# Optimization experiments

Measured on AMD Instinct MI355X. Metric: run time of the kernel, lower is better.

## Reference

```python
import jax, jax.numpy as jnp
import numpy as np

H, C = 4, 32            # heads, per-head channels
HID = H * C             # 128
IN_DIM, OUT_DIM = 300, 4
N, E = 50000, 800000
TE = HID // H           # time-encode dim = 32
EDGE_DIM = 2 * TE + 3   # 67
L = 2                   # num_layers


def setup_inputs() -> dict:
    key = jax.random.key(0)
    ks = jax.random.split(key, 20)
    p = lambda k, shape: jax.random.normal(k, shape, jnp.float32) * 0.02
    return {
        "x": jax.random.normal(ks[0], (N, IN_DIM), jnp.float32),
        "ei_td": jax.random.randint(ks[1], (2, E), 0, N),
        "ei_bu": jax.random.randint(ks[2], (2, E), 0, N),
        "ea_td": jax.random.uniform(ks[3], (E, 4), jnp.float32),
        "ea_bu": jax.random.uniform(ks[4], (E, 4), jnp.float32),
        "W_in": p(ks[5], (IN_DIM, HID)), "b_in": jnp.zeros((HID,), jnp.float32),
        "te_w": jax.random.uniform(ks[6], (TE,), jnp.float32),
        # stacked TransformerConv params: [layer, etype(TD,BU), ...]
        "Wq": p(ks[7], (L, 2, HID, HID)), "bq": jnp.zeros((L, 2, HID), jnp.float32),
        "Wk": p(ks[8], (L, 2, HID, HID)), "bk": jnp.zeros((L, 2, HID), jnp.float32),
        "Wv": p(ks[9], (L, 2, HID, HID)), "bv": jnp.zeros((L, 2, HID), jnp.float32),
        "We": p(ks[10], (L, 2, EDGE_DIM, HID)),  # lin_edge has no bias in PyG
        "Wskip": p(ks[11], (L, 2, HID, HID)), "bskip": jnp.zeros((L, 2, HID), jnp.float32),
        "gamma": jnp.ones((L, HID), jnp.float32), "beta": jnp.zeros((L, HID), jnp.float32),
        "W_out": p(ks[12], ((L + 1) * HID, OUT_DIM)), "b_out": jnp.zeros((OUT_DIM,), jnp.float32),
        "W_dec": p(ks[13], (HID, IN_DIM)), "b_dec": jnp.zeros((IN_DIM,), jnp.float32),
    }


def _edge_enc(ea, te_w):
    # TimeEncode on dt_norm, then [sin, cos, w_norm, infl_flag, cos_sim]
    ft = ea[:, 1:2] * te_w  # [E, TE]
    return jnp.concatenate([jnp.sin(ft), jnp.cos(ft), ea[:, 0:1], ea[:, 2:3], ea[:, 3:4]], axis=1)


def _tconv(h, src, dst, enc, Wq, bq, Wk, bk, Wv, bv, We, Wskip, bskip):
    # PyG TransformerConv (concat=True, root_weight=True, beta=False)
    n = h.shape[0]
    q = (h @ Wq + bq).reshape(n, H, C)
    k = (h @ Wk + bk).reshape(n, H, C)
    v = (h @ Wv + bv).reshape(n, H, C)
    e = (enc @ We).reshape(-1, H, C)                 # per-edge key/value offset
    ke = k[src] + e                                  # [E,H,C]
    alpha = jnp.einsum('ehc,ehc->eh', q[dst], ke) / jnp.sqrt(jnp.float32(C))
    amax = jax.ops.segment_max(alpha, dst, num_segments=n)     # scatter-softmax
    ex = jnp.exp(alpha - amax[dst])
    den = jax.ops.segment_sum(ex, dst, num_segments=n)
    a = ex / (den[dst] + 1e-16)                      # [E,H]
    msg = (v[src] + e) * a[:, :, None]
    out = jax.ops.segment_sum(msg, dst, num_segments=n).reshape(n, HID)
    return out + h @ Wskip + bskip                   # root/skip connection


def _ln(x, g, b):
    mu = jnp.mean(x, axis=-1, keepdims=True)
    var = jnp.mean((x - mu) ** 2, axis=-1, keepdims=True)
    return (x - mu) / jnp.sqrt(var + 1e-5) * g + b


def reference(x, ei_td, ei_bu, ea_td, ea_bu, W_in, b_in, te_w,
              Wq, bq, Wk, bk, Wv, bv, We, Wskip, bskip,
              gamma, beta, W_out, b_out, W_dec, b_dec):
    h = jax.nn.relu(x @ W_in + b_in)
    outs = [h]
    enc_td = _edge_enc(ea_td, te_w)
    enc_bu = _edge_enc(ea_bu, te_w)
    for i in range(L):
        o_td = _tconv(h, ei_td[0], ei_td[1], enc_td,
                      Wq[i, 0], bq[i, 0], Wk[i, 0], bk[i, 0], Wv[i, 0], bv[i, 0],
                      We[i, 0], Wskip[i, 0], bskip[i, 0])
        o_bu = _tconv(h, ei_bu[0], ei_bu[1], enc_bu,
                      Wq[i, 1], bq[i, 1], Wk[i, 1], bk[i, 1], Wv[i, 1], bv[i, 1],
                      We[i, 1], Wskip[i, 1], bskip[i, 1])
        t = jax.nn.relu(o_td + o_bu)                 # HeteroConv aggr='sum'; dropout=eval noop
        h = _ln(t, gamma[i], beta[i])
        outs.append(h)
    out = jnp.concatenate(outs, axis=1) @ W_out + b_out   # JumpingKnowledge 'cat'
    z = outs[-1]
    x_rec = z @ W_dec + b_dec
    return (out, z, x_rec)
```

## Files before the change

kernel.cpp:

```cpp
#include <hip/hip_runtime.h>

#define HID 128
#define CH 32
#define DPAD 68
#define PSTR 272
#define INDIM 300

typedef __attribute__((ext_vector_type(8))) short short8v;
typedef __attribute__((ext_vector_type(4))) short short4v;
typedef __attribute__((ext_vector_type(4))) float float4v;

__device__ __forceinline__ unsigned bf16_rne(float f){
  unsigned u = __float_as_uint(f);
  return (u + 0x7fffu + ((u >> 16) & 1u)) >> 16;
}
__device__ __forceinline__ void split_bf16(float f, short& hi, short& lo){
  unsigned h = bf16_rne(f);
  float fh = __uint_as_float(h << 16);
  unsigned l = bf16_rne(f - fh);
  hi = (short)h; lo = (short)l;
}
__device__ __forceinline__ int invperm32(int s31){
  return ((s31 >> 2) & 1) * 16 + ((s31 >> 3) & 3) * 4 + (s31 & 3);
}

__global__ void k_hist(const int* __restrict__ ei, int E, int* __restrict__ deg){
  int i = blockIdx.x*256 + threadIdx.x;
  if(i < E) atomicAdd(&deg[ei[E + i]], 1);
}

__global__ void k_scan(const int* __restrict__ deg, int n, int* __restrict__ seg, int* __restrict__ cur){
  __shared__ int wsum[16];
  __shared__ int wpre[16];
  int t = threadIdx.x;
  int wv = t >> 6, ln = t & 63;
  int running = 0;
  for(int base = 0; base < n; base += 8192){
    int vloc[8]; int idx0 = base + t*8;
    int s8 = 0;
    #pragma unroll
    for(int j=0;j<8;j++){ int ii = idx0+j; int d = (ii<n)? deg[ii] : 0; vloc[j] = s8; s8 += d; }
    int inc = s8;
    #pragma unroll
    for(int off=1; off<64; off<<=1){
      int y = __shfl_up(inc, off, 64);
      if (ln >= off) inc += y;
    }
    if (ln == 63) wsum[wv] = inc;
    __syncthreads();
    if (t < 16){
      int v = wsum[t];
      #pragma unroll
      for(int off=1; off<16; off<<=1){
        int y = __shfl_up(v, off, 64);
        if (t >= off) v += y;
      }
      wpre[t] = v;
    }
    __syncthreads();
    int wbase = (wv==0) ? 0 : wpre[wv-1];
    int excl = wbase + inc - s8;
    #pragma unroll
    for(int j=0;j<8;j++){
      int ii = idx0+j;
      if(ii<n){ int val = running + excl + vloc[j]; seg[ii]=val; cur[ii]=val; }
    }
    int total = wpre[15];
    __syncthreads();
    running += total;
  }
  if (t==0) seg[n] = running;
}

__global__ void k_scatter(const int* __restrict__ ei, const float* __restrict__ ea, int E,
                          int* __restrict__ cur, int* __restrict__ srcs, float4* __restrict__ eas){
  int i = blockIdx.x*256 + threadIdx.x;
  if(i >= E) return;
  int d = ei[E + i];
  int pos = atomicAdd(&cur[d], 1);
  srcs[pos] = ei[i];
  eas[pos] = ((const float4*)ea)[i];
}

__global__ void k_split(const float* __restrict__ W, short* __restrict__ bh, short* __restrict__ bl,
                        int K, int N, int Kpad, int Npad){
  int idx = blockIdx.x*256 + threadIdx.x;
  if (idx >= Npad*Kpad) return;
  int n = idx / Kpad, s = idx - n*Kpad;
  int k = (s & ~31) + invperm32(s & 31);
  float v = (n < N && k < K) ? W[(size_t)k*N + n] : 0.f;
  short hi, lo; split_bf16(v, hi, lo);
  bh[idx] = hi; bl[idx] = lo;
}

__global__ void k_split4(const float* __restrict__ W0, const float* __restrict__ W1,
                         const float* __restrict__ W2, const float* __restrict__ W3,
                         short* __restrict__ bh, short* __restrict__ bl){
  int slab = blockIdx.y;
  const float* W = (slab==0)?W0:(slab==1)?W1:(slab==2)?W2:W3;
  int idx = blockIdx.x*256 + threadIdx.x;
  int n = idx >> 7, s = idx & 127;
  int k = (s & ~31) + invperm32(s & 31);
  float v = W[k*HID + n];
  short hi, lo; split_bf16(v, hi, lo);
  bh[slab*16384 + idx] = hi; bl[slab*16384 + idx] = lo;
}

__global__ void k_wqwe_s(const float* __restrict__ Wq, const float* __restrict__ We,
                         short* __restrict__ bh, short* __restrict__ bl){
  int idx = blockIdx.x*256 + threadIdx.x;
  if (idx >= 384*128) return;
  int n = idx >> 7, s = idx & 127;
  int k = (s & ~31) + invperm32(s & 31);
  float v = 0.f;
  if (n < PSTR){
    int h = n / DPAD, d = n - h*DPAD;
    if (d < 67){
      const float* wr = Wq + k*HID + h*CH;
      const float* er = We + d*HID + h*CH;
      #pragma unroll
      for(int c=0;c<CH;c++) v += wr[c]*er[c];
    }
  }
  short hi, lo; split_bf16(v, hi, lo);
  bh[idx]=hi; bl[idx]=lo;
}

__global__ void k_pbias(const float* __restrict__ bq, const float* __restrict__ We, float* __restrict__ pbv){
  int n = blockIdx.x*256 + threadIdx.x;
  if (n >= PSTR) return;
  int h = n / DPAD, d = n - h*DPAD;
  float v = 0.f;
  if (d < 67){
    #pragma unroll
    for(int c=0;c<CH;c++) v += bq[h*CH+c]*We[d*HID + h*CH + c];
  }
  pbv[n] = v;
}

__global__ void k_weexp_s(const float* __restrict__ We, short* __restrict__ bh, short* __restrict__ bl){
  int idx = blockIdx.x*256 + threadIdx.x;
  if (idx >= 128*320) return;
  int n = idx / 320, s = idx - n*320;
  int k = (s & ~31) + invperm32(s & 31);
  float v = 0.f;
  if (k < PSTR){
    int h = k / DPAD, d = k - h*DPAD;
    if (d < 67 && (n>>5)==h) v = We[d*HID + n];
  }
  short hi, lo; split_bf16(v, hi, lo);
  bh[idx]=hi; bl[idx]=lo;
}

__global__ __launch_bounds__(256,2) void k_gemm(const float* __restrict__ A,
        const short* __restrict__ Bh, const short* __restrict__ Bl,
        const float* __restrict__ bias, float* __restrict__ C,
        int M, int N, int K, int Kpad, int mode){
  __shared__ short Ash[64*64], Asl[64*64];
  __shared__ short Bsh[128*64], Bsl[128*64];
  int tid = threadIdx.x;
  int l = tid & 63, w = tid >> 6;
  int lr = l & 15, q = l >> 4;
  int row0 = blockIdx.x*64, col0 = blockIdx.y*128;
  float4v acc[4][2];
  #pragma unroll
  for(int mt=0;mt<4;mt++){
    #pragma unroll
    for(int nt=0;nt<2;nt++) acc[mt][nt] = (float4v){0.f,0.f,0.f,0.f};
  }
  for (int k0 = 0; k0 < Kpad; k0 += 64){
    #pragma unroll
    for (int i=0;i<4;i++){
      int c = tid + i*256;
      int row = c >> 4, kq = c & 15;
      int gr = row0 + row, gk = k0 + kq*4;
      float4 a4 = make_float4(0.f,0.f,0.f,0.f);
      if (gr < M && gk < K) a4 = *(const float4*)(A + (size_t)gr*K + gk);
      short h0,h1,h2,h3,l0,l1,l2,l3;
      split_bf16(a4.x,h0,l0); split_bf16(a4.y,h1,l1);
      split_bf16(a4.z,h2,l2); split_bf16(a4.w,h3,l3);
      int cb = ((kq>>3)*64 + (kq&3)*16 + ((kq>>2)&1)*8) ^ ((row&7)<<4);
      int ih = row*64 + (cb>>1);
      *(short4v*)&Ash[ih] = (short4v){h0,h1,h2,h3};
      *(short4v*)&Asl[ih] = (short4v){l0,l1,l2,l3};
    }
    #pragma unroll
    for (int i=0;i<4;i++){
      int c = tid + i*256;
      int n = c >> 3, c8 = c & 7;
      size_t gidx = (size_t)(col0 + n)*Kpad + k0 + c8*8;
      int cb = (c8*16) ^ ((n&7)<<4);
      int ih = n*64 + (cb>>1);
      *(short8v*)&Bsh[ih] = *(const short8v*)(Bh + gidx);
      *(short8v*)&Bsl[ih] = *(const short8v*)(Bl + gidx);
    }
    __syncthreads();
    #pragma unroll
    for (int ks=0; ks<2; ks++){
      short8v ah[4], al[4], bh[2], bl[2];
      #pragma unroll
      for (int mt=0; mt<4; mt++){
        int r = mt*16 + lr;
        int cb = (ks*64 + q*16) ^ ((r&7)<<4);
        int ih = r*64 + (cb>>1);
        ah[mt] = *(const short8v*)&Ash[ih];
        al[mt] = *(const short8v*)&Asl[ih];
      }
      #pragma unroll
      for (int nt=0; nt<2; nt++){
        int r = w*32 + nt*16 + lr;
        int cb = (ks*64 + q*16) ^ ((r&7)<<4);
        int ih = r*64 + (cb>>1);
        bh[nt] = *(const short8v*)&Bsh[ih];
        bl[nt] = *(const short8v*)&Bsl[ih];
      }
      #pragma unroll
      for (int mt=0; mt<4; mt++){
        #pragma unroll
        for (int nt=0; nt<2; nt++){
          acc[mt][nt] = __builtin_amdgcn_mfma_f32_16x16x32_bf16(ah[mt], bh[nt], acc[mt][nt], 0,0,0);
          acc[mt][nt] = __builtin_amdgcn_mfma_f32_16x16x32_bf16(ah[mt], bl[nt], acc[mt][nt], 0,0,0);
          acc[mt][nt] = __builtin_amdgcn_mfma_f32_16x16x32_bf16(al[mt], bh[nt], acc[mt][nt], 0,0,0);
        }
      }
    }
    __syncthreads();
  }
  #pragma unroll
  for (int mt=0; mt<4; mt++){
    #pragma unroll
    for (int nt=0; nt<2; nt++){
      int gc = col0 + w*32 + nt*16 + lr;
      if (gc >= N) continue;
      float bv = bias ? bias[gc] : 0.f;
      #pragma unroll
      for (int r=0; r<4; r++){
        int gr = row0 + mt*16 + q*4 + r;
        if (gr >= M) continue;
        float v = acc[mt][nt][r] + bv;
        float* cp = C + (size_t)gr*N + gc;
        if (mode==1) v = fmaxf(v, 0.f);
        if (mode==2) v += *cp;
        *cp = v;
      }
    }
  }
}

__global__ __launch_bounds__(256) void k_attn(const float* __restrict__ q, const float* __restrict__ k,
      const float* __restrict__ v, const float* __restrict__ P,
      const int* __restrict__ srcs, const float4* __restrict__ eas,
      const int* __restrict__ seg, const float* __restrict__ tw,
      float* __restrict__ acc, float* __restrict__ S, float* __restrict__ abuf, int Nn){
  __shared__ float als[4][1024];
  int tid = threadIdx.x;
  int wv = tid >> 6;
  int wid = (blockIdx.x * 256 + tid) >> 6;
  int lane = tid & 63;
  if(wid >= Nn) return;
  int beg = seg[wid], end = seg[wid+1];
  int g = lane >> 4, l = lane & 15;
  int hown = l >> 2;
  const float* qp = q + (size_t)wid*HID + l*8;
  float4 qa = *(const float4*)qp, qb4 = *(const float4*)(qp+4);
  float qv[8] = {qa.x,qa.y,qa.z,qa.w,qb4.x,qb4.y,qb4.z,qb4.w};
  float Pr[4][4], Pt[4];
  #pragma unroll
  for(int h=0;h<4;h++){
    float4 pv = *(const float4*)(P + (size_t)wid*PSTR + h*DPAD + l*4);
    Pr[h][0]=pv.x; Pr[h][1]=pv.y; Pr[h][2]=pv.z; Pr[h][3]=pv.w;
    Pt[h] = (l<4) ? P[(size_t)wid*PSTR + h*DPAD + 64 + l] : 0.f;
  }
  float twv[4];
  #pragma unroll
  for(int t=0;t<4;t++) twv[t] = tw[((l&7)<<2) + t];
  bool issin = (l < 8);
  float mx[4] = {-3.4e38f,-3.4e38f,-3.4e38f,-3.4e38f};
  for(int e0 = beg; e0 < end; e0 += 4){
    int e = e0 + g;
    bool valid = (e < end);
    float p[4] = {0.f,0.f,0.f,0.f};
    if(valid){
      int src = srcs[e];
      const float* kp = k + (size_t)src*HID + l*8;
      float4 ka = *(const float4*)kp, kb4 = *(const float4*)(kp+4);
      float qk = qv[0]*ka.x + qv[1]*ka.y + qv[2]*ka.z + qv[3]*ka.w
               + qv[4]*kb4.x + qv[5]*kb4.y + qv[6]*kb4.z + qv[7]*kb4.w;
      p[hown] = qk;
      float4 ea4 = eas[e];
      float ea1 = ea4.y;
      float ec[4];
      #pragma unroll
      for(int t=0;t<4;t++){
        float ft = ea1 * twv[t];
        ec[t] = issin ? __sinf(ft) : __cosf(ft);
      }
      #pragma unroll
      for(int h=0;h<4;h++){
        #pragma unroll
        for(int t=0;t<4;t++) p[h] += ec[t]*Pr[h][t];
      }
      if(l < 4){
        float et = (l==0)? ea4.x : (l==1)? ea4.z : (l==2)? ea4.w : 0.f;
        #pragma unroll
        for(int h=0;h<4;h++) p[h] += et*Pt[h];
      }
    }
    #pragma unroll
    for(int m=1;m<16;m<<=1){
      #pragma unroll
      for(int h=0;h<4;h++) p[h] += __shfl_xor(p[h], m, 64);
    }
    if(valid){
      #pragma unroll
      for(int h=0;h<4;h++){
        float a = p[h]*0.17677669529663687f;
        p[h] = a;
        mx[h] = fmaxf(mx[h], a);
      }
      if(l < 4){
        int off = e - beg;
        if (off < 256) als[wv][off*4 + l] = p[l];
        else           abuf[(size_t)e*4 + l] = p[l];
      }
    }
  }
  #pragma unroll
  for(int m=16;m<64;m<<=1){
    #pragma unroll
    for(int h=0;h<4;h++) mx[h] = fmaxf(mx[h], __shfl_xor(mx[h], m, 64));
  }
  float accv[8] = {0.f,0.f,0.f,0.f,0.f,0.f,0.f,0.f};
  float accS[4][4] = {{0.f}};
  float accT[4] = {0.f,0.f,0.f,0.f};
  float den[4] = {0.f,0.f,0.f,0.f};
  for(int e0 = beg; e0 < end; e0 += 4){
    int e = e0 + g;
    if(e < end){
      int off = e - beg;
      float4 a4 = (off < 256) ? *(const float4*)&als[wv][off*4]
                              : *(const float4*)(abuf + (size_t)e*4);
      float eh[4];
      eh[0] = __expf(a4.x - mx[0]); eh[1] = __expf(a4.y - mx[1]);
      eh[2] = __expf(a4.z - mx[2]); eh[3] = __expf(a4.w - mx[3]);
      if(l == 0){
        #pragma unroll
        for(int h=0;h<4;h++) den[h] += eh[h];
      }
      int src = srcs[e];
      const float* vp = v + (size_t)src*HID + l*8;
      float4 va = *(const float4*)vp, vb4 = *(const float4*)(vp+4);
      float vv[8] = {va.x,va.y,va.z,va.w,vb4.x,vb4.y,vb4.z,vb4.w};
      float eo = eh[hown];
      #pragma unroll
      for(int j=0;j<8;j++) accv[j] += eo*vv[j];
      float4 ea4 = eas[e]; float ea1 = ea4.y;
      float ec[4];
      #pragma unroll
      for(int t=0;t<4;t++){
        float ft = ea1 * twv[t];
        ec[t] = issin ? __sinf(ft) : __cosf(ft);
      }
      #pragma unroll
      for(int h=0;h<4;h++){
        #pragma unroll
        for(int t=0;t<4;t++) accS[h][t] += eh[h]*ec[t];
      }
      if(l < 4){
        float et = (l==0)? ea4.x : (l==1)? ea4.z : (l==2)? ea4.w : 0.f;
        #pragma unroll
        for(int h=0;h<4;h++) accT[h] += eh[h]*et;
      }
    }
  }
  #pragma unroll
  for(int m=1;m<64;m<<=1){
    #pragma unroll
    for(int h=0;h<4;h++) den[h] += __shfl_xor(den[h], m, 64);
  }
  #pragma unroll
  for(int m=16;m<64;m<<=1){
    #pragma unroll
    for(int j=0;j<8;j++) accv[j] += __shfl_xor(accv[j], m, 64);
    #pragma unroll
    for(int h=0;h<4;h++){
      #pragma unroll
      for(int t=0;t<4;t++) accS[h][t] += __shfl_xor(accS[h][t], m, 64);
      accT[h] += __shfl_xor(accT[h], m, 64);
    }
  }
  float rden[4];
  #pragma unroll
  for(int h=0;h<4;h++) rden[h] = 1.f / (den[h] + 1e-16f);
  if(g == 0){
    float ro = rden[hown];
    float* op = acc + (size_t)wid*HID + l*8;
    float4 o0 = *(const float4*)op, o1 = *(const float4*)(op+4);
    *(float4*)op     = make_float4(o0.x+accv[0]*ro, o0.y+accv[1]*ro, o0.z+accv[2]*ro, o0.w+accv[3]*ro);
    *(float4*)(op+4) = make_float4(o1.x+accv[4]*ro, o1.y+accv[5]*ro, o1.z+accv[6]*ro, o1.w+accv[7]*ro);
    #pragma unroll
    for(int h=0;h<4;h++){
      *(float4*)(S + (size_t)wid*PSTR + h*DPAD + l*4) =
          make_float4(accS[h][0]*rden[h],accS[h][1]*rden[h],accS[h][2]*rden[h],accS[h][3]*rden[h]);
    }
    if(l < 4){
      #pragma unroll
      for(int h=0;h<4;h++) S[(size_t)wid*PSTR + h*DPAD + 64 + l] = accT[h]*rden[h];
    }
  }
}

__global__ __launch_bounds__(256) void k_ln(const float* __restrict__ acc,
   const float* __restrict__ gamma, const float* __restrict__ beta,
   float* __restrict__ hout, int Nn){
  int wid = (blockIdx.x*blockDim.x + threadIdx.x) >> 6;
  int lane = threadIdx.x & 63;
  if(wid >= Nn) return;
  size_t b = (size_t)wid*HID;
  int c0 = lane, c1 = lane + 64;
  float t0 = fmaxf(acc[b+c0], 0.f);
  float t1 = fmaxf(acc[b+c1], 0.f);
  float s = t0+t1, ss = t0*t0+t1*t1;
  #pragma unroll
  for(int m=1;m<64;m<<=1){ s += __shfl_xor(s,m,64); ss += __shfl_xor(ss,m,64); }
  float mu = s * (1.f/128.f);
  float var = ss*(1.f/128.f) - mu*mu;
  float rstd = 1.f / sqrtf(var + 1e-5f);
  hout[b+c0] = (t0-mu)*rstd*gamma[c0] + beta[c0];
  hout[b+c1] = (t1-mu)*rstd*gamma[c1] + beta[c1];
}

__global__ __launch_bounds__(256) void k_out4(const float* __restrict__ h0, const float* __restrict__ h1,
    const float* __restrict__ h2, const float* __restrict__ Wout, const float* __restrict__ bout,
    float* __restrict__ out, int Nn){
  __shared__ float Wl[384*4];
  int tid = threadIdx.x;
  #pragma unroll
  for(int i=0;i<6;i++) Wl[tid + i*256] = Wout[tid + i*256];
  __syncthreads();
  int wid = (blockIdx.x*256 + tid) >> 6;
  int lane = tid & 63;
  if(wid >= Nn) return;
  float p0=0.f,p1=0.f,p2=0.f,p3=0.f;
  #pragma unroll
  for(int ch=0; ch<6; ch++){
    int kidx = ch*64 + lane;
    const float* hs = (kidx < 128) ? h0 : (kidx < 256) ? h1 : h2;
    float x = hs[(size_t)wid*HID + (kidx & 127)];
    float4 w4 = *(const float4*)&Wl[kidx*4];
    p0 += x*w4.x; p1 += x*w4.y; p2 += x*w4.z; p3 += x*w4.w;
  }
  #pragma unroll
  for(int m=1;m<64;m<<=1){
    p0 += __shfl_xor(p0,m,64); p1 += __shfl_xor(p1,m,64);
    p2 += __shfl_xor(p2,m,64); p3 += __shfl_xor(p3,m,64);
  }
  if(lane < 4){
    float pv = (lane==0)?p0:(lane==1)?p1:(lane==2)?p2:p3;
    out[(size_t)wid*4 + lane] = pv + bout[lane];
  }
}

extern "C" void kernel_launch(void* const* d_in, const int* in_sizes, int n_in,
                              void* d_out, int out_size, void* d_ws, size_t ws_size,
                              hipStream_t stream) {
  const float* x    = (const float*)d_in[0];
  const int*   ei_td= (const int*)d_in[1];
  const int*   ei_bu= (const int*)d_in[2];
  const float* ea_td= (const float*)d_in[3];
  const float* ea_bu= (const float*)d_in[4];
  const float* W_in = (const float*)d_in[5];
  const float* b_in = (const float*)d_in[6];
  const float* te_w = (const float*)d_in[7];
  const float* Wq   = (const float*)d_in[8];
  const float* bq   = (const float*)d_in[9];
  const float* Wk   = (const float*)d_in[10];
  const float* bk   = (const float*)d_in[11];
  const float* Wv   = (const float*)d_in[12];
  const float* bv   = (const float*)d_in[13];
  const float* We   = (const float*)d_in[14];
  const float* Wsk  = (const float*)d_in[15];
  const float* bsk  = (const float*)d_in[16];
  const float* gamma= (const float*)d_in[17];
  const float* beta = (const float*)d_in[18];
  const float* Wout = (const float*)d_in[19];
  const float* bout = (const float*)d_in[20];
  const float* Wdec = (const float*)d_in[21];
  const float* bdec = (const float*)d_in[22];
  (void)n_in; (void)out_size; (void)ws_size;

  int Nn = in_sizes[0] / INDIM;
  int Et = in_sizes[1] / 2;
  int Eb = in_sizes[2] / 2;

  float* outF = (float*)d_out;
  float* z_reg    = outF + (size_t)Nn*4;
  float* xrec_reg = z_reg + (size_t)Nn*HID;
  float* vb   = z_reg;
  float* Pbuf = xrec_reg;
  float* tail = xrec_reg + (size_t)Nn*PSTR;
  float* pbv  = tail;            tail += PSTR;
  int* seg_td = (int*)tail;      tail += Nn+1;
  int* seg_bu = (int*)tail;      tail += Nn+1;
  int* cur    = (int*)tail;      tail += Nn;
  int* deg    = (int*)tail;      tail += Nn;

  char* p = (char*)d_ws;
  auto alloc = [&](size_t bytes)->void*{ void* r = (void*)p; p += (bytes + 255) & ~(size_t)255; return r; };
  float* outs0 = (float*)alloc((size_t)Nn*HID*4);
  float* outs1 = (float*)alloc((size_t)Nn*HID*4);
  float* qb    = (float*)alloc((size_t)Nn*HID*4);
  float* kb    = (float*)alloc((size_t)Nn*HID*4);
  float* accb  = (float*)alloc((size_t)Nn*HID*4);
  int   Emax   = (Et > Eb) ? Et : Eb;
  float* abuf  = (float*)alloc((size_t)Emax*4*4);
  int* srcs_td = (int*)alloc((size_t)Et*4);
  int* srcs_bu = (int*)alloc((size_t)Eb*4);
  float* eas_td= (float*)alloc((size_t)Et*4*4);
  float* eas_bu= (float*)alloc((size_t)Eb*4*4);
  short* bt4_h = (short*)alloc(65536*2);
  short* bt4_l = (short*)alloc(65536*2);
  short* btP_h = (short*)alloc(49152*2);
  short* btP_l = (short*)alloc(49152*2);
  short* btE_h = (short*)alloc(40960*2);
  short* btE_l = (short*)alloc(40960*2);
  short* btG_h = (short*)alloc(49152*2);
  short* btG_l = (short*)alloc(49152*2);

  hipMemsetAsync(deg, 0, (size_t)Nn*4, stream);
  k_hist<<<(Et+255)/256, 256, 0, stream>>>(ei_td, Et, deg);
  k_scan<<<1, 1024, 0, stream>>>(deg, Nn, seg_td, cur);
  k_scatter<<<(Et+255)/256, 256, 0, stream>>>(ei_td, ea_td, Et, cur, srcs_td, (float4*)eas_td);

  hipMemsetAsync(deg, 0, (size_t)Nn*4, stream);
  k_hist<<<(Eb+255)/256, 256, 0, stream>>>(ei_bu, Eb, deg);
  k_scan<<<1, 1024, 0, stream>>>(deg, Nn, seg_bu, cur);
  k_scatter<<<(Eb+255)/256, 256, 0, stream>>>(ei_bu, ea_bu, Eb, cur, srcs_bu, (float4*)eas_bu);

  int gM = (Nn + 63) / 64;
  k_split<<<(128*320+255)/256, 256, 0, stream>>>(W_in, btG_h, btG_l, INDIM, HID, 320, 128);
  k_gemm<<<dim3(gM,1), 256, 0, stream>>>(x, btG_h, btG_l, b_in, outs0, Nn, HID, INDIM, 320, 1);

  float* hbuf[3] = {outs0, outs1, z_reg};
  for(int i = 0; i < 2; i++){
    const float* h = hbuf[i];
    hipMemsetAsync(accb, 0, (size_t)Nn*HID*4, stream);
    for(int et = 0; et < 2; et++){
      int wi = i*2 + et;
      const float* Wq_ = Wq + (size_t)wi*HID*HID; const float* bq_ = bq + (size_t)wi*HID;
      const float* Wk_ = Wk + (size_t)wi*HID*HID; const float* bk_ = bk + (size_t)wi*HID;
      const float* Wv_ = Wv + (size_t)wi*HID*HID; const float* bv_ = bv + (size_t)wi*HID;
      const float* Ws_ = Wsk+ (size_t)wi*HID*HID; const float* bs_ = bsk+ (size_t)wi*HID;
      const float* We_ = We + (size_t)wi*67*HID;
      const int* seg  = et ? seg_bu : seg_td;
      const int* srcs = et ? srcs_bu : srcs_td;
      const float* eas= et ? eas_bu : eas_td;

      k_split4<<<dim3(64,4), 256, 0, stream>>>(Wq_, Wk_, Wv_, Ws_, bt4_h, bt4_l);
      k_wqwe_s<<<192, 256, 0, stream>>>(Wq_, We_, btP_h, btP_l);
      k_pbias<<<2, 256, 0, stream>>>(bq_, We_, pbv);
      k_weexp_s<<<160, 256, 0, stream>>>(We_, btE_h, btE_l);

      k_gemm<<<dim3(gM,1), 256, 0, stream>>>(h, bt4_h,           bt4_l,           bq_, qb, Nn, HID, HID, HID, 0);
      k_gemm<<<dim3(gM,1), 256, 0, stream>>>(h, bt4_h + 16384,   bt4_l + 16384,   bk_, kb, Nn, HID, HID, HID, 0);
      k_gemm<<<dim3(gM,1), 256, 0, stream>>>(h, bt4_h + 32768,   bt4_l + 32768,   bv_, vb, Nn, HID, HID, HID, 0);
      k_gemm<<<dim3(gM,3), 256, 0, stream>>>(h, btP_h,           btP_l,           pbv, Pbuf, Nn, PSTR, HID, HID, 0);
      k_attn<<<(Nn*64+255)/256, 256, 0, stream>>>(qb, kb, vb, Pbuf, srcs, (const float4*)eas,
                                                  seg, te_w, accb, Pbuf, abuf, Nn);
      k_gemm<<<dim3(gM,1), 256, 0, stream>>>(Pbuf, btE_h,        btE_l,           nullptr, accb, Nn, HID, PSTR, 320, 2);
      k_gemm<<<dim3(gM,1), 256, 0, stream>>>(h, bt4_h + 49152,   bt4_l + 49152,   bs_, accb, Nn, HID, HID, HID, 2);
    }
    k_ln<<<(Nn*64+255)/256, 256, 0, stream>>>(accb, gamma + (size_t)i*HID, beta + (size_t)i*HID,
                                              hbuf[i+1], Nn);
  }

  k_out4<<<(Nn*64+255)/256, 256, 0, stream>>>(outs0, outs1, z_reg, Wout, bout, outF, Nn);
  k_split<<<(384*128+255)/256, 256, 0, stream>>>(Wdec, btG_h, btG_l, HID, INDIM, 128, 384);
  k_gemm<<<dim3(gM,3), 256, 0, stream>>>(z_reg, btG_h, btG_l, bdec, xrec_reg, Nn, INDIM, HID, 128, 0);
}
```

Measured before the change: 2.129 ms.

## Fuse QKV+skip GEMM, store K/V as bf16, single-pass online-softmax attention

```diff
diff --git a/kernel.cpp b/kernel.cpp
--- a/kernel.cpp
+++ b/kernel.cpp
@@ -5,6 +5,7 @@
 #define DPAD 68
 #define PSTR 272
 #define INDIM 300
+#define QROW 384
 
 typedef __attribute__((ext_vector_type(8))) short short8v;
 typedef __attribute__((ext_vector_type(4))) short short4v;
@@ -19,6 +20,9 @@
   float fh = __uint_as_float(h << 16);
   unsigned l = bf16_rne(f - fh);
   hi = (short)h; lo = (short)l;
+}
+__device__ __forceinline__ float b2f(short s){
+  return __uint_as_float(((unsigned)(unsigned short)s) << 16);
 }
 __device__ __forceinline__ int invperm32(int s31){
   return ((s31 >> 2) & 1) * 16 + ((s31 >> 3) & 3) * 4 + (s31 & 3);
@@ -152,10 +156,28 @@
   bh[idx]=hi; bl[idx]=lo;
 }
 
-__global__ __launch_bounds__(256,2) void k_gemm(const float* __restrict__ A,
+__global__ void k_bias4(const float* __restrict__ b0, const float* __restrict__ b1,
+                        const float* __restrict__ b2, const float* __restrict__ b3,
+                        float* __restrict__ out){
+  int t = blockIdx.x*256 + threadIdx.x;
+  if (t >= 512) return;
+  float v = (t<128)? b0[t] : (t<256)? b1[t-128] : (t<384)? b2[t-256] : b3[t-384];
+  out[t] = v;
+}
+
+__global__ void k_splitA(const float* __restrict__ A, short* __restrict__ ah, short* __restrict__ al, int total){
+  int i = blockIdx.x*256 + threadIdx.x;
+  if (i >= total) return;
+  short hi, lo; split_bf16(A[i], hi, lo);
+  ah[i]=hi; al[i]=lo;
+}
+
+__global__ __launch_bounds__(256,2) void k_gemm(
+        const short* __restrict__ Ah, const short* __restrict__ Al, const float* __restrict__ Af,
         const short* __restrict__ Bh, const short* __restrict__ Bl,
         const float* __restrict__ bias, float* __restrict__ C,
-        int M, int N, int K, int Kpad, int mode){
+        short* __restrict__ Ch, short* __restrict__ Cl,
+        int M, int N, int K, int Ks, int Kpad, int mode){
   __shared__ short Ash[64*64], Asl[64*64];
   __shared__ short Bsh[128*64], Bsl[128*64];
   int tid = threadIdx.x;
@@ -169,20 +191,38 @@
     for(int nt=0;nt<2;nt++) acc[mt][nt] = (float4v){0.f,0.f,0.f,0.f};
   }
   for (int k0 = 0; k0 < Kpad; k0 += 64){
-    #pragma unroll
-    for (int i=0;i<4;i++){
-      int c = tid + i*256;
-      int row = c >> 4, kq = c & 15;
-      int gr = row0 + row, gk = k0 + kq*4;
-      float4 a4 = make_float4(0.f,0.f,0.f,0.f);
-      if (gr < M && gk < K) a4 = *(const float4*)(A + (size_t)gr*K + gk);
-      short h0,h1,h2,h3,l0,l1,l2,l3;
-      split_bf16(a4.x,h0,l0); split_bf16(a4.y,h1,l1);
-      split_bf16(a4.z,h2,l2); split_bf16(a4.w,h3,l3);
-      int cb = ((kq>>3)*64 + (kq&3)*16 + ((kq>>2)&1)*8) ^ ((row&7)<<4);
-      int ih = row*64 + (cb>>1);
-      *(short4v*)&Ash[ih] = (short4v){h0,h1,h2,h3};
-      *(short4v*)&Asl[ih] = (short4v){l0,l1,l2,l3};
+    if (Af){
+      #pragma unroll
+      for (int i=0;i<4;i++){
+        int c = tid + i*256;
+        int row = c >> 4, kq = c & 15;
+        int gr = row0 + row, gk = k0 + kq*4;
+        float4 a4 = make_float4(0.f,0.f,0.f,0.f);
+        if (gr < M && gk < K) a4 = *(const float4*)(Af + (size_t)gr*Ks + gk);
+        short h0,h1,h2,h3,l0,l1,l2,l3;
+        split_bf16(a4.x,h0,l0); split_bf16(a4.y,h1,l1);
+        split_bf16(a4.z,h2,l2); split_bf16(a4.w,h3,l3);
+        int cb = ((kq>>3)*64 + (kq&3)*16 + ((kq>>2)&1)*8) ^ ((row&7)<<4);
+        int ih = row*64 + (cb>>1);
+        *(short4v*)&Ash[ih] = (short4v){h0,h1,h2,h3};
+        *(short4v*)&Asl[ih] = (short4v){l0,l1,l2,l3};
+      }
+    } else {
+      #pragma unroll
+      for (int i=0;i<4;i++){
+        int c = tid + i*256;
+        int row = c >> 4, kq = c & 15;
+        int gr = row0 + row, gk = k0 + kq*4;
+        short4v a4h = (short4v){0,0,0,0}, a4l = (short4v){0,0,0,0};
+        if (gr < M && gk < K){
+          a4h = *(const short4v*)(Ah + (size_t)gr*Ks + gk);
+          a4l = *(const short4v*)(Al + (size_t)gr*Ks + gk);
+        }
+        int cb = ((kq>>3)*64 + (kq&3)*16 + ((kq>>2)&1)*8) ^ ((row&7)<<4);
+        int ih = row*64 + (cb>>1);
+        *(short4v*)&Ash[ih] = a4h;
+        *(short4v*)&Asl[ih] = a4l;
+      }
     }
     #pragma unroll
     for (int i=0;i<4;i++){
@@ -226,43 +266,50 @@
     }
     __syncthreads();
   }
+  short* qs = (short*)C;
   #pragma unroll
   for (int mt=0; mt<4; mt++){
     #pragma unroll
     for (int nt=0; nt<2; nt++){
       int gc = col0 + w*32 + nt*16 + lr;
-      if (gc >= N) continue;
+      if (mode != 3 && gc >= N) continue;
       float bv = bias ? bias[gc] : 0.f;
       #pragma unroll
       for (int r=0; r<4; r++){
         int gr = row0 + mt*16 + q*4 + r;
         if (gr >= M) continue;
         float v = acc[mt][nt][r] + bv;
-        float* cp = C + (size_t)gr*N + gc;
-        if (mode==1) v = fmaxf(v, 0.f);
-        if (mode==2) v += *cp;
-        *cp = v;
-      }
-    }
-  }
-}
-
-__global__ __launch_bounds__(256) void k_attn(const float* __restrict__ q, const float* __restrict__ k,
-      const float* __restrict__ v, const float* __restrict__ P,
+        if (mode == 3){
+          if (gc < 256) C[(size_t)gr*QROW + gc] = v;
+          else          qs[(size_t)gr*(QROW*2) + 256 + gc] = (short)bf16_rne(v);
+        } else if (mode == 4){
+          v = fmaxf(v, 0.f);
+          short hi, lo; split_bf16(v, hi, lo);
+          Ch[(size_t)gr*N + gc] = hi;
+          Cl[(size_t)gr*N + gc] = lo;
+        } else {
+          float* cp = C + (size_t)gr*N + gc;
+          if (mode == 2) v += *cp;
+          *cp = v;
+        }
+      }
+    }
+  }
+}
+
+__global__ __launch_bounds__(256) void k_attn(const float* __restrict__ qkvs, const float* __restrict__ P,
       const int* __restrict__ srcs, const float4* __restrict__ eas,
       const int* __restrict__ seg, const float* __restrict__ tw,
-      float* __restrict__ acc, float* __restrict__ S, float* __restrict__ abuf, int Nn){
-  __shared__ float als[4][1024];
+      float* __restrict__ acc, float* __restrict__ S, int Nn, int addmode){
   int tid = threadIdx.x;
-  int wv = tid >> 6;
   int wid = (blockIdx.x * 256 + tid) >> 6;
   int lane = tid & 63;
   if(wid >= Nn) return;
   int beg = seg[wid], end = seg[wid+1];
   int g = lane >> 4, l = lane & 15;
   int hown = l >> 2;
-  const float* qp = q + (size_t)wid*HID + l*8;
-  float4 qa = *(const float4*)qp, qb4 = *(const float4*)(qp+4);
+  const float* rowq = qkvs + (size_t)wid*QROW;
+  float4 qa = *(const float4*)(rowq + l*8), qb4 = *(const float4*)(rowq + l*8 + 4);
   float qv[8] = {qa.x,qa.y,qa.z,qa.w,qb4.x,qb4.y,qb4.z,qb4.w};
   float Pr[4][4], Pt[4];
   #pragma unroll
@@ -275,17 +322,22 @@
   #pragma unroll
   for(int t=0;t<4;t++) twv[t] = tw[((l&7)<<2) + t];
   bool issin = (l < 8);
-  float mx[4] = {-3.4e38f,-3.4e38f,-3.4e38f,-3.4e38f};
+  float mx[4] = {-3.0e38f,-3.0e38f,-3.0e38f,-3.0e38f};
+  float den[4] = {0.f,0.f,0.f,0.f};
+  float accv[8] = {0.f,0.f,0.f,0.f,0.f,0.f,0.f,0.f};
+  float accS[4][4] = {{0.f}};
+  float accT[4] = {0.f,0.f,0.f,0.f};
   for(int e0 = beg; e0 < end; e0 += 4){
     int e = e0 + g;
-    bool valid = (e < end);
-    float p[4] = {0.f,0.f,0.f,0.f};
-    if(valid){
+    if(e < end){
       int src = srcs[e];
-      const float* kp = k + (size_t)src*HID + l*8;
-      float4 ka = *(const float4*)kp, kb4 = *(const float4*)(kp+4);
-      float qk = qv[0]*ka.x + qv[1]*ka.y + qv[2]*ka.z + qv[3]*ka.w
-               + qv[4]*kb4.x + qv[5]*kb4.y + qv[6]*kb4.z + qv[7]*kb4.w;
+      const short* kvp = (const short*)(qkvs + (size_t)src*QROW) + 512 + l*8;
+      short8v k8 = *(const short8v*)kvp;
+      short8v v8 = *(const short8v*)(kvp + 128);
+      float qk = 0.f;
+      #pragma unroll
+      for(int j=0;j<8;j++) qk += qv[j]*b2f(k8[j]);
+      float p[4] = {0.f,0.f,0.f,0.f};
       p[hown] = qk;
       float4 ea4 = eas[e];
       float ea1 = ea4.y;
@@ -300,86 +352,67 @@
         #pragma unroll
         for(int t=0;t<4;t++) p[h] += ec[t]*Pr[h][t];
       }
+      float et = 0.f;
       if(l < 4){
-        float et = (l==0)? ea4.x : (l==1)? ea4.z : (l==2)? ea4.w : 0.f;
+        et = (l==0)? ea4.x : (l==1)? ea4.z : (l==2)? ea4.w : 0.f;
         #pragma unroll
         for(int h=0;h<4;h++) p[h] += et*Pt[h];
       }
-    }
-    #pragma unroll
-    for(int m=1;m<16;m<<=1){
-      #pragma unroll
-      for(int h=0;h<4;h++) p[h] += __shfl_xor(p[h], m, 64);
-    }
-    if(valid){
+      #pragma unroll
+      for(int m=1;m<16;m<<=1){
+        #pragma unroll
+        for(int h=0;h<4;h++) p[h] += __shfl_xor(p[h], m, 64);
+      }
+      float eh[4], fs[4];
       #pragma unroll
       for(int h=0;h<4;h++){
         float a = p[h]*0.17677669529663687f;
-        p[h] = a;
-        mx[h] = fmaxf(mx[h], a);
-      }
-      if(l < 4){
-        int off = e - beg;
-        if (off < 256) als[wv][off*4 + l] = p[l];
-        else           abuf[(size_t)e*4 + l] = p[l];
-      }
-    }
-  }
-  #pragma unroll
-  for(int m=16;m<64;m<<=1){
-    #pragma unroll
-    for(int h=0;h<4;h++) mx[h] = fmaxf(mx[h], __shfl_xor(mx[h], m, 64));
-  }
-  float accv[8] = {0.f,0.f,0.f,0.f,0.f,0.f,0.f,0.f};
-  float accS[4][4] = {{0.f}};
-  float accT[4] = {0.f,0.f,0.f,0.f};
-  float den[4] = {0.f,0.f,0.f,0.f};
-  for(int e0 = beg; e0 < end; e0 += 4){
-    int e = e0 + g;
-    if(e < end){
-      int off = e - beg;
-      float4 a4 = (off < 256) ? *(const float4*)&als[wv][off*4]
-                              : *(const float4*)(abuf + (size_t)e*4);
-      float eh[4];
-      eh[0] = __expf(a4.x - mx[0]); eh[1] = __expf(a4.y - mx[1]);
-      eh[2] = __expf(a4.z - mx[2]); eh[3] = __expf(a4.w - mx[3]);
-      if(l == 0){
-        #pragma unroll
-        for(int h=0;h<4;h++) den[h] += eh[h];
-      }
-      int src = srcs[e];
-      const float* vp = v + (size_t)src*HID + l*8;
-      float4 va = *(const float4*)vp, vb4 = *(const float4*)(vp+4);
-      float vv[8] = {va.x,va.y,va.z,va.w,vb4.x,vb4.y,vb4.z,vb4.w};
-      float eo = eh[hown];
-      #pragma unroll
-      for(int j=0;j<8;j++) accv[j] += eo*vv[j];
-      float4 ea4 = eas[e]; float ea1 = ea4.y;
-      float ec[4];
-      #pragma unroll
-      for(int t=0;t<4;t++){
-        float ft = ea1 * twv[t];
-        ec[t] = issin ? __sinf(ft) : __cosf(ft);
-      }
+        float nm = fmaxf(mx[h], a);
+        fs[h] = __expf(mx[h] - nm);
+        eh[h] = __expf(a - nm);
+        den[h] = den[h]*fs[h] + eh[h];
+        mx[h] = nm;
+      }
+      float fo = fs[hown], eo = eh[hown];
+      #pragma unroll
+      for(int j=0;j<8;j++) accv[j] = accv[j]*fo + eo*b2f(v8[j]);
       #pragma unroll
       for(int h=0;h<4;h++){
         #pragma unroll
-        for(int t=0;t<4;t++) accS[h][t] += eh[h]*ec[t];
+        for(int t=0;t<4;t++) accS[h][t] = accS[h][t]*fs[h] + eh[h]*ec[t];
       }
       if(l < 4){
-        float et = (l==0)? ea4.x : (l==1)? ea4.z : (l==2)? ea4.w : 0.f;
         #pragma unroll
-        for(int h=0;h<4;h++) accT[h] += eh[h]*et;
-      }
-    }
-  }
-  #pragma unroll
-  for(int m=1;m<64;m<<=1){
+        for(int h=0;h<4;h++) accT[h] = accT[h]*fs[h] + eh[h]*et;
+      }
+    }
+  }
+  float gm[4], cf[4];
+  #pragma unroll
+  for(int h=0;h<4;h++) gm[h] = mx[h];
+  #pragma unroll
+  for(int m=16;m<64;m<<=1){
+    #pragma unroll
+    for(int h=0;h<4;h++) gm[h] = fmaxf(gm[h], __shfl_xor(gm[h], m, 64));
+  }
+  #pragma unroll
+  for(int h=0;h<4;h++){
+    cf[h] = __expf(mx[h] - gm[h]);
+    den[h] *= cf[h];
+  }
+  float co = cf[hown];
+  #pragma unroll
+  for(int j=0;j<8;j++) accv[j] *= co;
+  #pragma unroll
+  for(int h=0;h<4;h++){
+    #pragma unroll
+    for(int t=0;t<4;t++) accS[h][t] *= cf[h];
+    accT[h] *= cf[h];
+  }
+  #pragma unroll
+  for(int m=16;m<64;m<<=1){
     #pragma unroll
     for(int h=0;h<4;h++) den[h] += __shfl_xor(den[h], m, 64);
-  }
-  #pragma unroll
-  for(int m=16;m<64;m<<=1){
     #pragma unroll
     for(int j=0;j<8;j++) accv[j] += __shfl_xor(accv[j], m, 64);
     #pragma unroll
@@ -394,10 +427,19 @@
   for(int h=0;h<4;h++) rden[h] = 1.f / (den[h] + 1e-16f);
   if(g == 0){
     float ro = rden[hown];
+    float4 s0 = *(const float4*)(rowq + 128 + l*8);
+    float4 s1 = *(const float4*)(rowq + 128 + l*8 + 4);
+    float o[8];
+    o[0]=accv[0]*ro+s0.x; o[1]=accv[1]*ro+s0.y; o[2]=accv[2]*ro+s0.z; o[3]=accv[3]*ro+s0.w;
+    o[4]=accv[4]*ro+s1.x; o[5]=accv[5]*ro+s1.y; o[6]=accv[6]*ro+s1.z; o[7]=accv[7]*ro+s1.w;
     float* op = acc + (size_t)wid*HID + l*8;
-    float4 o0 = *(const float4*)op, o1 = *(const float4*)(op+4);
-    *(float4*)op     = make_float4(o0.x+accv[0]*ro, o0.y+accv[1]*ro, o0.z+accv[2]*ro, o0.w+accv[3]*ro);
-    *(float4*)(op+4) = make_float4(o1.x+accv[4]*ro, o1.y+accv[5]*ro, o1.z+accv[6]*ro, o1.w+accv[7]*ro);
+    if (addmode){
+      float4 a0 = *(const float4*)op, a1 = *(const float4*)(op+4);
+      o[0]+=a0.x; o[1]+=a0.y; o[2]+=a0.z; o[3]+=a0.w;
+      o[4]+=a1.x; o[5]+=a1.y; o[6]+=a1.z; o[7]+=a1.w;
+    }
+    *(float4*)op     = make_float4(o[0],o[1],o[2],o[3]);
+    *(float4*)(op+4) = make_float4(o[4],o[5],o[6],o[7]);
     #pragma unroll
     for(int h=0;h<4;h++){
       *(float4*)(S + (size_t)wid*PSTR + h*DPAD + l*4) =
@@ -412,7 +454,7 @@
 
 __global__ __launch_bounds__(256) void k_ln(const float* __restrict__ acc,
    const float* __restrict__ gamma, const float* __restrict__ beta,
-   float* __restrict__ hout, int Nn){
+   float* __restrict__ hout, short* __restrict__ Hh, short* __restrict__ Hl, int Nn){
   int wid = (blockIdx.x*blockDim.x + threadIdx.x) >> 6;
   int lane = threadIdx.x & 63;
   if(wid >= Nn) return;
@@ -426,12 +468,18 @@
   float mu = s * (1.f/128.f);
   float var = ss*(1.f/128.f) - mu*mu;
   float rstd = 1.f / sqrtf(var + 1e-5f);
-  hout[b+c0] = (t0-mu)*rstd*gamma[c0] + beta[c0];
-  hout[b+c1] = (t1-mu)*rstd*gamma[c1] + beta[c1];
-}
-
-__global__ __launch_bounds__(256) void k_out4(const float* __restrict__ h0, const float* __restrict__ h1,
-    const float* __restrict__ h2, const float* __restrict__ Wout, const float* __restrict__ bout,
+  float y0 = (t0-mu)*rstd*gamma[c0] + beta[c0];
+  float y1 = (t1-mu)*rstd*gamma[c1] + beta[c1];
+  hout[b+c0] = y0; hout[b+c1] = y1;
+  short h0,l0,h1,l1;
+  split_bf16(y0,h0,l0); split_bf16(y1,h1,l1);
+  Hh[b+c0]=h0; Hl[b+c0]=l0;
+  Hh[b+c1]=h1; Hl[b+c1]=l1;
+}
+
+__global__ __launch_bounds__(256) void k_out4(const short* __restrict__ H0h, const short* __restrict__ H0l,
+    const short* __restrict__ H1h, const short* __restrict__ H1l, const float* __restrict__ z,
+    const float* __restrict__ Wout, const float* __restrict__ bout,
     float* __restrict__ out, int Nn){
   __shared__ float Wl[384*4];
   int tid = threadIdx.x;
@@ -445,8 +493,16 @@
   #pragma unroll
   for(int ch=0; ch<6; ch++){
     int kidx = ch*64 + lane;
-    const float* hs = (kidx < 128) ? h0 : (kidx < 256) ? h1 : h2;
-    float x = hs[(size_t)wid*HID + (kidx & 127)];
+    float x;
+    if (kidx < 128){
+      size_t ix = (size_t)wid*HID + kidx;
+      x = b2f(H0h[ix]) + b2f(H0l[ix]);
+    } else if (kidx < 256){
+      size_t ix = (size_t)wid*HID + (kidx-128);
+      x = b2f(H1h[ix]) + b2f(H1l[ix]);
+    } else {
+      x = z[(size_t)wid*HID + (kidx-256)];
+    }
     float4 w4 = *(const float4*)&Wl[kidx*4];
     p0 += x*w4.x; p1 += x*w4.y; p2 += x*w4.z; p3 += x*w4.w;
   }
@@ -496,10 +552,9 @@
   float* outF = (float*)d_out;
   float* z_reg    = outF + (size_t)Nn*4;
   float* xrec_reg = z_reg + (size_t)Nn*HID;
-  float* vb   = z_reg;
+  float* accb = z_reg;
   float* Pbuf = xrec_reg;
   float* tail = xrec_reg + (size_t)Nn*PSTR;
-  float* pbv  = tail;            tail += PSTR;
   int* seg_td = (int*)tail;      tail += Nn+1;
   int* seg_bu = (int*)tail;      tail += Nn+1;
   int* cur    = (int*)tail;      tail += Nn;
@@ -507,25 +562,29 @@
 
   char* p = (char*)d_ws;
   auto alloc = [&](size_t bytes)->void*{ void* r = (void*)p; p += (bytes + 255) & ~(size_t)255; return r; };
-  float* outs0 = (float*)alloc((size_t)Nn*HID*4);
-  float* outs1 = (float*)alloc((size_t)Nn*HID*4);
-  float* qb    = (float*)alloc((size_t)Nn*HID*4);
-  float* kb    = (float*)alloc((size_t)Nn*HID*4);
-  float* accb  = (float*)alloc((size_t)Nn*HID*4);
-  int   Emax   = (Et > Eb) ? Et : Eb;
-  float* abuf  = (float*)alloc((size_t)Emax*4*4);
+  float* qkvs  = (float*)alloc((size_t)Nn*QROW*4);
+  short* H0h   = (short*)alloc((size_t)Nn*HID*2);
+  short* H0l   = (short*)alloc((size_t)Nn*HID*2);
+  short* H1h   = (short*)alloc((size_t)Nn*HID*2);
+  short* H1l   = (short*)alloc((size_t)Nn*HID*2);
   int* srcs_td = (int*)alloc((size_t)Et*4);
   int* srcs_bu = (int*)alloc((size_t)Eb*4);
   float* eas_td= (float*)alloc((size_t)Et*4*4);
   float* eas_bu= (float*)alloc((size_t)Eb*4*4);
-  short* bt4_h = (short*)alloc(65536*2);
-  short* bt4_l = (short*)alloc(65536*2);
+  short* btQ_h = (short*)alloc(65536*2);
+  short* btQ_l = (short*)alloc(65536*2);
   short* btP_h = (short*)alloc(49152*2);
   short* btP_l = (short*)alloc(49152*2);
   short* btE_h = (short*)alloc(40960*2);
   short* btE_l = (short*)alloc(40960*2);
   short* btG_h = (short*)alloc(49152*2);
   short* btG_l = (short*)alloc(49152*2);
+  float* qbias = (float*)alloc(512*4);
+  float* pbv   = (float*)alloc(PSTR*4);
+  short* xh = (short*)qkvs;
+  short* xl = xh + (size_t)Nn*INDIM;
+  short* Zh = (short*)qkvs;
+  short* Zl = Zh + (size_t)Nn*HID;
 
   hipMemsetAsync(deg, 0, (size_t)Nn*4, stream);
   k_hist<<<(Et+255)/256, 256, 0, stream>>>(ei_td, Et, deg);
@@ -538,13 +597,14 @@
   k_scatter<<<(Eb+255)/256, 256, 0, stream>>>(ei_bu, ea_bu, Eb, cur, srcs_bu, (float4*)eas_bu);
 
   int gM = (Nn + 63) / 64;
+  k_splitA<<<((Nn*INDIM)+255)/256, 256, 0, stream>>>(x, xh, xl, Nn*INDIM);
   k_split<<<(128*320+255)/256, 256, 0, stream>>>(W_in, btG_h, btG_l, INDIM, HID, 320, 128);
-  k_gemm<<<dim3(gM,1), 256, 0, stream>>>(x, btG_h, btG_l, b_in, outs0, Nn, HID, INDIM, 320, 1);
-
-  float* hbuf[3] = {outs0, outs1, z_reg};
+  k_gemm<<<dim3(gM,1), 256, 0, stream>>>(xh, xl, nullptr, btG_h, btG_l, b_in,
+        nullptr, H0h, H0l, Nn, HID, INDIM, INDIM, 320, 4);
+
   for(int i = 0; i < 2; i++){
-    const float* h = hbuf[i];
-    hipMemsetAsync(accb, 0, (size_t)Nn*HID*4, stream);
+    const short* Hh = (i==0)? H0h : H1h;
+    const short* Hl = (i==0)? H0l : H1l;
     for(int et = 0; et < 2; et++){
       int wi = i*2 + et;
       const float* Wq_ = Wq + (size_t)wi*HID*HID; const float* bq_ = bq + (size_t)wi*HID;
@@ -556,25 +616,29 @@
       const int* srcs = et ? srcs_bu : srcs_td;
       const float* eas= et ? eas_bu : eas_td;
 
-      k_split4<<<dim3(64,4), 256, 0, stream>>>(Wq_, Wk_, Wv_, Ws_, bt4_h, bt4_l);
+      k_split4<<<dim3(64,4), 256, 0, stream>>>(Wq_, Ws_, Wk_, Wv_, btQ_h, btQ_l);
+      k_bias4<<<2, 256, 0, stream>>>(bq_, bs_, bk_, bv_, qbias);
       k_wqwe_s<<<192, 256, 0, stream>>>(Wq_, We_, btP_h, btP_l);
       k_pbias<<<2, 256, 0, stream>>>(bq_, We_, pbv);
       k_weexp_s<<<160, 256, 0, stream>>>(We_, btE_h, btE_l);
 
-      k_gemm<<<dim3(gM,1), 256, 0, stream>>>(h, bt4_h,           bt4_l,           bq_, qb, Nn, HID, HID, HID, 0);
-      k_gemm<<<dim3(gM,1), 256, 0, stream>>>(h, bt4_h + 16384,   bt4_l + 16384,   bk_, kb, Nn, HID, HID, HID, 0);
-      k_gemm<<<dim3(gM,1), 256, 0, stream>>>(h, bt4_h + 32768,   bt4_l + 32768,   bv_, vb, Nn, HID, HID, HID, 0);
-      k_gemm<<<dim3(gM,3), 256, 0, stream>>>(h, btP_h,           btP_l,           pbv, Pbuf, Nn, PSTR, HID, HID, 0);
-      k_attn<<<(Nn*64+255)/256, 256, 0, stream>>>(qb, kb, vb, Pbuf, srcs, (const float4*)eas,
-                                                  seg, te_w, accb, Pbuf, abuf, Nn);
-      k_gemm<<<dim3(gM,1), 256, 0, stream>>>(Pbuf, btE_h,        btE_l,           nullptr, accb, Nn, HID, PSTR, 320, 2);
-      k_gemm<<<dim3(gM,1), 256, 0, stream>>>(h, bt4_h + 49152,   bt4_l + 49152,   bs_, accb, Nn, HID, HID, HID, 2);
-    }
-    k_ln<<<(Nn*64+255)/256, 256, 0, stream>>>(accb, gamma + (size_t)i*HID, beta + (size_t)i*HID,
-                                              hbuf[i+1], Nn);
-  }
-
-  k_out4<<<(Nn*64+255)/256, 256, 0, stream>>>(outs0, outs1, z_reg, Wout, bout, outF, Nn);
+      k_gemm<<<dim3(gM,4), 256, 0, stream>>>(Hh, Hl, nullptr, btQ_h, btQ_l, qbias,
+            qkvs, nullptr, nullptr, Nn, 512, HID, HID, HID, 3);
+      k_gemm<<<dim3(gM,3), 256, 0, stream>>>(Hh, Hl, nullptr, btP_h, btP_l, pbv,
+            Pbuf, nullptr, nullptr, Nn, PSTR, HID, HID, HID, 0);
+      k_attn<<<(Nn*64+255)/256, 256, 0, stream>>>(qkvs, Pbuf, srcs, (const float4*)eas,
+                                                  seg, te_w, accb, Pbuf, Nn, et);
+      k_gemm<<<dim3(gM,1), 256, 0, stream>>>(nullptr, nullptr, Pbuf, btE_h, btE_l, nullptr,
+            accb, nullptr, nullptr, Nn, HID, PSTR, PSTR, 320, 2);
+    }
+    if (i == 0)
+      k_ln<<<(Nn*64+255)/256, 256, 0, stream>>>(accb, gamma, beta, z_reg, H1h, H1l, Nn);
+    else
+      k_ln<<<(Nn*64+255)/256, 256, 0, stream>>>(accb, gamma + HID, beta + HID, z_reg, Zh, Zl, Nn);
+  }
+
+  k_out4<<<(Nn*64+255)/256, 256, 0, stream>>>(H0h, H0l, H1h, H1l, z_reg, Wout, bout, outF, Nn);
   k_split<<<(384*128+255)/256, 256, 0, stream>>>(Wdec, btG_h, btG_l, HID, INDIM, 128, 384);
-  k_gemm<<<dim3(gM,3), 256, 0, stream>>>(z_reg, btG_h, btG_l, bdec, xrec_reg, Nn, INDIM, HID, 128, 0);
-}
+  k_gemm<<<dim3(gM,3), 256, 0, stream>>>(Zh, Zl, nullptr, btG_h, btG_l, bdec,
+        xrec_reg, nullptr, nullptr, Nn, INDIM, HID, HID, 128, 0);
+}
```

New measurement: 1.969 ms. 7.5% less time.
